# Kernel tuning notes

Hardware: AMD Instinct MI355X
Metric: run time of the kernel (lower is better)

The kernel has to match this reference:

```python
import jax, jax.numpy as jnp
import numpy as np
import math

DIM = 1024
H = 16
DH = DIM // H
B = 2
L = 1024


def setup_inputs() -> dict:
    key = jax.random.key(0)
    ks = jax.random.split(key, 8)
    s = 1.0 / math.sqrt(DIM)
    return {
        "Q": jax.random.normal(ks[0], (B, L, DIM), jnp.float32),
        "K": jax.random.normal(ks[1], (B, L, DIM), jnp.float32),
        "mask_Q": jax.random.bernoulli(ks[2], 0.1, (B, L)),
        "mask_K": jax.random.bernoulli(ks[3], 0.1, (B, L)),
        "Wq": jax.random.normal(ks[4], (DIM, DIM), jnp.float32) * s,
        "Wk": jax.random.normal(ks[5], (DIM, DIM), jnp.float32) * s,
        "Wv": jax.random.normal(ks[6], (DIM, DIM), jnp.float32) * s,
        "Wo": jax.random.normal(ks[7], (DIM, DIM), jnp.float32) * s,
    }


def reference(Q, K, mask_Q, mask_K, Wq, Wk, Wv, Wo):
    # V defaults to K. Masked positions of inputs are zeroed first.
    Qz = jnp.where(mask_Q[:, :, None], 0.0, Q)
    Kz = jnp.where(mask_K[:, :, None], 0.0, K)
    Vz = Kz  # V = K, masked with mask_K

    # Projections (nn.Linear, no bias): y = x @ W.T
    Qp = jnp.einsum('bld,ed->ble', Qz, Wq)
    Kp = jnp.einsum('bld,ed->ble', Kz, Wk)
    Vp = jnp.einsum('bld,ed->ble', Vz, Wv)

    # split heads: [B, L, H, DH] -> per-head attention
    qh = Qp.reshape(B, L, H, DH)
    kh = Kp.reshape(B, L, H, DH)
    vh = Vp.reshape(B, L, H, DH)

    # NOTE: original scales by sqrt(dim) (full dim), not sqrt(dim_split)
    scores = jnp.einsum('bqhd,bkhd->bhqk', qh, kh) / math.sqrt(DIM)

    # outer-product validity mask: valid iff both q and k positions unmasked
    valid = (~mask_Q)[:, None, :, None] & (~mask_K)[:, None, None, :]  # [B,1,Lq,Lk]
    A = jnp.where(valid, scores, -1e38)
    A = jax.nn.softmax(A, axis=-1)
    A = jnp.where(valid, A, 0.0)

    O = jnp.einsum('bhqk,bkhd->bqhd', A, vh).reshape(B, L, DIM)
    # residual uses the PROJECTED Q (Q was reassigned to fc_q(Q) in torch)
    O = Qp + O
    # masked_forward(fc_o, ...): fc_o applied, masked query rows forced to 0
    ff = jax.nn.relu(jnp.where(mask_Q[:, :, None], 0.0, jnp.einsum('bld,ed->ble', O, Wo)))
    O = O + ff
    return O
```

## Files before the change

### kernel.cpp

```cpp
#include <hip/hip_runtime.h>
#include <hip/hip_bf16.h>


#define DEV __device__ __forceinline__

typedef __attribute__((ext_vector_type(8))) short bf16x8;
typedef __attribute__((ext_vector_type(4))) float f32x4;
typedef __hip_bfloat16 bf16;

DEV void glds16(const bf16* g, bf16* s) {
  __builtin_amdgcn_global_load_lds(
      (const __attribute__((address_space(1))) void*)g,
      (__attribute__((address_space(3))) void*)s, 16, 0, 0);
}

DEV unsigned short f2bu(float x) {
  __hip_bfloat16 b = __float2bfloat16(x);
  unsigned short u;
  __builtin_memcpy(&u, &b, 2);
  return u;
}

__global__ void normalize_masks(const unsigned char* mq_raw, const unsigned char* mk_raw,
                                unsigned char* outq, unsigned char* outk,
                                unsigned long long* qm64, unsigned long long* km64) {
  __shared__ int cnt;
  int t = threadIdx.x;
  if (t == 0) cnt = 0;
  __syncthreads();
  int c = 0;
  for (int i = t; i < 2048; i += 256) c += (mq_raw[i] != 0);
  atomicAdd(&cnt, c);
  __syncthreads();
  bool isByte = cnt > 128;
  for (int i = t; i < 2048; i += 256) {
    unsigned char q, k;
    if (isByte) {
      q = (mq_raw[i] != 0); k = (mk_raw[i] != 0);
    } else {
      q = (((const int*)mq_raw)[i] != 0); k = (((const int*)mk_raw)[i] != 0);
    }
    outq[i] = q; outk[i] = k;
  }
  __syncthreads();
  if (t < 64) {
    const unsigned char* src = (t < 32) ? outk : outq;
    int idx = t & 31;
    unsigned long long m = 0;
    for (int j = 0; j < 64; ++j)
      m |= (unsigned long long)(src[idx * 64 + j] != 0) << j;
    if (t < 32) km64[idx] = m; else qm64[idx] = m;
  }
}

__global__ __launch_bounds__(256) void cast_all(
    const float* __restrict__ Q, const float* __restrict__ K,
    const unsigned char* __restrict__ mq, const unsigned char* __restrict__ mk,
    const float* __restrict__ W0, const float* __restrict__ W1,
    const float* __restrict__ W2, const float* __restrict__ W3,
    bf16* __restrict__ Qz, bf16* __restrict__ Kz,
    bf16* __restrict__ o0, bf16* __restrict__ o1,
    bf16* __restrict__ o2, bf16* __restrict__ o3) {
  const int z = blockIdx.z;
  if (z < 2) {
    const float* X = z ? K : Q;
    const unsigned char* m = z ? mk : mq;
    bf16* out = z ? Kz : Qz;
    int i = (blockIdx.x * 256 + threadIdx.x) * 8;
    float4 v0 = *(const float4*)&X[i];
    float4 v1 = *(const float4*)&X[i + 4];
    if (m[i >> 10]) {
      v0 = make_float4(0.f, 0.f, 0.f, 0.f);
      v1 = make_float4(0.f, 0.f, 0.f, 0.f);
    }
    *(ushort4*)&out[i] = make_ushort4(f2bu(v0.x), f2bu(v0.y), f2bu(v0.z), f2bu(v0.w));
    *(ushort4*)&out[i + 4] = make_ushort4(f2bu(v1.x), f2bu(v1.y), f2bu(v1.z), f2bu(v1.w));
  } else {
    const float* X; bf16* out;
    switch (z) {
      case 2: X = W0; out = o0; break;
      case 3: X = W1; out = o1; break;
      case 4: X = W2; out = o2; break;
      default: X = W3; out = o3; break;
    }
    int i = (blockIdx.x * 256 + threadIdx.x) * 4;
    float4 v = *(const float4*)&X[i];
    *(ushort4*)&out[i] = make_ushort4(f2bu(v.x), f2bu(v.y), f2bu(v.z), f2bu(v.w));
  }
}

template <int MI, typename EPI>
DEV void gemm_core(const bf16* __restrict__ A, const bf16* __restrict__ W,
                   int K, int brow, int bcol, EPI&& epi) {
  constexpr int BM = MI * 32;
  __shared__ bf16 As[2][BM * 32];
  __shared__ bf16 Bs[2][128 * 32];
  const int t = threadIdx.x, l = t & 63, w = t >> 6;
  const int wr = w >> 1, wc = w & 1;
  const int rs = l >> 2;
  const int kcol = (l & 3) * 8;

  f32x4 acc[MI][4];
#pragma unroll
  for (int i = 0; i < MI; i++)
#pragma unroll
    for (int j = 0; j < 4; j++) acc[i][j] = (f32x4){0.f, 0.f, 0.f, 0.f};

  const int aoff = (wr * (MI * 16) + (l & 15)) * 32 + (l >> 4) * 8;
  const int boff = (wc * 64 + (l & 15)) * 32 + (l >> 4) * 8;

  auto stage = [&](int k0, int b_) {
    if constexpr (MI == 4) {
#pragma unroll
      for (int c = 0; c < 2; ++c)
        glds16(A + (size_t)(brow + w * 32 + c * 16 + rs) * K + k0 + kcol,
               &As[b_][w * 1024 + c * 512]);
    } else {
      glds16(A + (size_t)(brow + w * 16 + rs) * K + k0 + kcol, &As[b_][w * 512]);
    }
#pragma unroll
    for (int c = 0; c < 2; ++c)
      glds16(W + (size_t)(bcol + w * 32 + c * 16 + rs) * K + k0 + kcol,
             &Bs[b_][w * 1024 + c * 512]);
  };

  stage(0, 0);
  int buf = 0;
  for (int k0 = 0; k0 < K; k0 += 32) {
    __syncthreads();
    if (k0 + 32 < K) stage(k0 + 32, buf ^ 1);
    bf16x8 a[MI], b[4];
#pragma unroll
    for (int mi = 0; mi < MI; ++mi) a[mi] = *(const bf16x8*)&As[buf][aoff + mi * 512];
#pragma unroll
    for (int ni = 0; ni < 4; ++ni) b[ni] = *(const bf16x8*)&Bs[buf][boff + ni * 512];
#pragma unroll
    for (int mi = 0; mi < MI; ++mi)
#pragma unroll
      for (int ni = 0; ni < 4; ++ni)
        acc[mi][ni] = __builtin_amdgcn_mfma_f32_16x16x32_bf16(a[mi], b[ni], acc[mi][ni], 0, 0, 0);
    buf ^= 1;
  }

#pragma unroll
  for (int mi = 0; mi < MI; ++mi)
#pragma unroll
    for (int ni = 0; ni < 4; ++ni)
#pragma unroll
      for (int r = 0; r < 4; ++r) {
        int row = brow + wr * (MI * 16) + mi * 16 + (l >> 4) * 4 + r;
        int col = bcol + wc * 64 + ni * 16 + (l & 15);
        epi(row, col, acc[mi][ni][r]);
      }
}

__global__ __launch_bounds__(256) void proj_gemm(
    const bf16* __restrict__ Qz, const bf16* __restrict__ Kz,
    const bf16* __restrict__ Wq, const bf16* __restrict__ Wk, const bf16* __restrict__ Wv,
    float* __restrict__ Qpf, bf16* __restrict__ Qpb,
    bf16* __restrict__ Kpb, bf16* __restrict__ Vpb) {
  const int z = blockIdx.z;
  const int brow = blockIdx.x * 128, bcol = blockIdx.y * 128;
  if (z == 0) {
    gemm_core<4>(Qz, Wq, 1024, brow, bcol, [&](int row, int col, float v) {
      size_t idx = (size_t)row * 1024 + col;
      Qpf[idx] = v;
      Qpb[idx] = __float2bfloat16(v * 0.045084220f);
    });
  } else if (z == 1) {
    gemm_core<4>(Kz, Wk, 1024, brow, bcol, [&](int row, int col, float v) {
      Kpb[(size_t)row * 1024 + col] = __float2bfloat16(v);
    });
  } else {
    gemm_core<4>(Kz, Wv, 1024, brow, bcol, [&](int row, int col, float v) {
      Vpb[(size_t)row * 1024 + col] = __float2bfloat16(v);
    });
  }
}

__global__ __launch_bounds__(256) void final_gemm(
    const bf16* __restrict__ Ob, const bf16* __restrict__ Wo,
    float* __restrict__ out, const unsigned char* __restrict__ mq) {
  const int brow = blockIdx.x * 64, bcol = blockIdx.y * 128;
  gemm_core<2>(Ob, Wo, 1024, brow, bcol, [&](int row, int col, float v) {
    size_t idx = (size_t)row * 1024 + col;
    float ff = mq[row] ? 0.f : fmaxf(v, 0.f);
    out[idx] = out[idx] + ff;
  });
}

__global__ __launch_bounds__(256) void attn_fused(
    const bf16* __restrict__ Qpb, const bf16* __restrict__ Kpb, const bf16* __restrict__ Vpb,
    const float* __restrict__ Qpf,
    const unsigned long long* __restrict__ qm64, const unsigned long long* __restrict__ km64,
    float* __restrict__ Of, bf16* __restrict__ Ob) {
  __shared__ bf16 Klds[2][64 * 64];
  __shared__ bf16 Vt[64 * 72];

  const int t = threadIdx.x, l = t & 63, w = t >> 6;
  const int q = l & 15, g = l >> 4;
  const int f = blockIdx.x;
  const int bh = (f & 7) + 8 * ((f >> 3) & 3);
  const int qt = f >> 5;
  const int b = bh >> 4, h = bh & 15;
  const size_t bbase = (size_t)b * 1024;

  const int qg = qt * 64 + w * 16 + q;
  const bf16* qptr = Qpb + (bbase + qg) * 1024 + h * 64 + g * 8;
  const bf16x8 qb0 = *(const bf16x8*)qptr;
  const bf16x8 qb1 = *(const bf16x8*)(qptr + 32);

  float psum = 0.f;
  f32x4 oacc[4];
#pragma unroll
  for (int mf = 0; mf < 4; ++mf) oacc[mf] = (f32x4){0.f, 0.f, 0.f, 0.f};

  const int krow_s = l >> 3;
  const int kcol_s = ((l & 7) ^ krow_s) * 8;
  const int vk0 = 2 * (t & 31);
  const int vdc = t >> 5;

  union { uint4 v; unsigned short s[8]; } u0, u1;

  auto stageK = [&](int kt_, int b_) {
#pragma unroll
    for (int c = 0; c < 2; ++c) {
      int cw = w * 2 + c;
      glds16(Kpb + (bbase + kt_ * 64 + cw * 8 + krow_s) * 1024 + h * 64 + kcol_s,
             &Klds[b_][cw * 512]);
    }
  };
  auto loadV = [&](int kt_) {
    const bf16* g0 = Vpb + (bbase + kt_ * 64 + vk0) * 1024 + h * 64 + vdc * 8;
    u0.v = *(const uint4*)g0;
    u1.v = *(const uint4*)(g0 + 1024);
  };

  stageK(0, 0);
  loadV(0);
  int buf = 0;

  for (int kt = 0; kt < 16; ++kt) {
    const unsigned long long km = km64[b * 16 + kt];
    const unsigned long long mloc = km >> (4 * g);

    __syncthreads();

#pragma unroll
    for (int j = 0; j < 8; ++j) {
      unsigned int pk = (unsigned int)u0.s[j] | ((unsigned int)u1.s[j] << 16);
      *(unsigned int*)((char*)Vt + (vdc * 8 + j) * 144 + vk0 * 2) = pk;
    }

    f32x4 S[4];
#pragma unroll
    for (int mf = 0; mf < 4; ++mf) {
#pragma unroll
      for (int r = 0; r < 4; ++r)
        S[mf][r] = ((mloc >> (mf * 16 + r)) & 1ull) ? -1e30f : 0.f;
      const int row = mf * 16 + q;
      const int rowb = row * 128;
      const bf16x8 ka0 = *(const bf16x8*)((const char*)&Klds[buf][0] + rowb + ((g ^ (row & 7)) * 16));
      const bf16x8 ka1 = *(const bf16x8*)((const char*)&Klds[buf][0] + rowb + (((g + 4) ^ (row & 7)) * 16));
      S[mf] = __builtin_amdgcn_mfma_f32_16x16x32_bf16(ka0, qb0, S[mf], 0, 0, 0);
      S[mf] = __builtin_amdgcn_mfma_f32_16x16x32_bf16(ka1, qb1, S[mf], 0, 0, 0);
    }

    unsigned int lo[4], hi[4];
#pragma unroll
    for (int mf = 0; mf < 4; ++mf) {
      float p0 = exp2f(S[mf][0]), p1 = exp2f(S[mf][1]);
      float p2 = exp2f(S[mf][2]), p3 = exp2f(S[mf][3]);
      psum += (p0 + p1) + (p2 + p3);
      lo[mf] = (unsigned int)f2bu(p0) | ((unsigned int)f2bu(p1) << 16);
      hi[mf] = (unsigned int)f2bu(p2) | ((unsigned int)f2bu(p3) << 16);
    }

    __syncthreads();

    if (kt < 15) {
      stageK(kt + 1, buf ^ 1);
      loadV(kt + 1);
    }

    const int srcA = ((2 * g) & 3) * 16 + q;
    const int srcB = srcA + 16;
    const bool sel = (g >> 1) & 1;
#pragma unroll
    for (int ks = 0; ks < 2; ++ks) {
      unsigned int a0 = __shfl(lo[2 * ks], srcA), a1 = __shfl(hi[2 * ks], srcA);
      unsigned int a2 = __shfl(lo[2 * ks], srcB), a3 = __shfl(hi[2 * ks], srcB);
      unsigned int b0 = __shfl(lo[2 * ks + 1], srcA), b1 = __shfl(hi[2 * ks + 1], srcA);
      unsigned int b2 = __shfl(lo[2 * ks + 1], srcB), b3 = __shfl(hi[2 * ks + 1], srcB);
      uint4 pw;
      pw.x = sel ? b0 : a0; pw.y = sel ? b1 : a1;
      pw.z = sel ? b2 : a2; pw.w = sel ? b3 : a3;
      const bf16x8 pa = __builtin_bit_cast(bf16x8, pw);
#pragma unroll
      for (int mf = 0; mf < 4; ++mf) {
        const bf16x8 va = *(const bf16x8*)((const char*)Vt + (mf * 16 + q) * 144 + ks * 64 + g * 16);
        oacc[mf] = __builtin_amdgcn_mfma_f32_16x16x32_bf16(va, pa, oacc[mf], 0, 0, 0);
      }
    }
    buf ^= 1;
  }

  psum += __shfl_xor(psum, 16);
  psum += __shfl_xor(psum, 32);

  const unsigned long long qm = qm64[b * 16 + qt];
  const bool qvalid = !((qm >> (w * 16 + q)) & 1ull);
  const float inv = (qvalid && psum > 0.f) ? 1.f / psum : 0.f;
#pragma unroll
  for (int mf = 0; mf < 4; ++mf) {
    size_t idx = (bbase + qg) * 1024 + h * 64 + mf * 16 + g * 4;
    float4 qp = *(const float4*)&Qpf[idx];
    float4 val;
    val.x = qp.x + oacc[mf][0] * inv;
    val.y = qp.y + oacc[mf][1] * inv;
    val.z = qp.z + oacc[mf][2] * inv;
    val.w = qp.w + oacc[mf][3] * inv;
    *(float4*)&Of[idx] = val;
    *(ushort4*)&Ob[idx] = make_ushort4(f2bu(val.x), f2bu(val.y), f2bu(val.z), f2bu(val.w));
  }
}

extern "C" void kernel_launch(void* const* d_in, const int* in_sizes, int n_in,
                              void* d_out, int out_size, void* d_ws, size_t ws_size,
                              hipStream_t stream) {
  const float* Q = (const float*)d_in[0];
  const float* K = (const float*)d_in[1];
  const unsigned char* mQraw = (const unsigned char*)d_in[2];
  const unsigned char* mKraw = (const unsigned char*)d_in[3];
  const float* Wq = (const float*)d_in[4];
  const float* Wk = (const float*)d_in[5];
  const float* Wv = (const float*)d_in[6];
  const float* Wo = (const float*)d_in[7];
  float* out = (float*)d_out;

  char* ws = (char*)d_ws;
  const size_t MB = 1024 * 1024;
  bf16* Qz = (bf16*)(ws + 0);
  bf16* Kz = (bf16*)(ws + 4 * MB);
  bf16* Wqb = (bf16*)(ws + 8 * MB);
  bf16* Wkb = (bf16*)(ws + 10 * MB);
  bf16* Wvb = (bf16*)(ws + 12 * MB);
  bf16* Wob = (bf16*)(ws + 14 * MB);
  float* Qpf = (float*)(ws + 16 * MB);
  bf16* Qpb = (bf16*)(ws + 24 * MB);
  bf16* Kpb = (bf16*)(ws + 28 * MB);
  bf16* Vpb = (bf16*)(ws + 32 * MB);
  bf16* Ob = (bf16*)(ws + 36 * MB);
  unsigned char* mqn = (unsigned char*)(ws + 40 * MB);
  unsigned char* mkn = mqn + 2048;
  unsigned long long* km64 = (unsigned long long*)(ws + 40 * MB + 4096);
  unsigned long long* qm64 = km64 + 32;

  normalize_masks<<<1, 256, 0, stream>>>(mQraw, mKraw, mqn, mkn, qm64, km64);

  dim3 gc(1024, 1, 6);
  cast_all<<<gc, 256, 0, stream>>>(Q, K, mqn, mkn, Wq, Wk, Wv, Wo,
                                   Qz, Kz, Wqb, Wkb, Wvb, Wob);

  dim3 gp(16, 8, 3);
  proj_gemm<<<gp, 256, 0, stream>>>(Qz, Kz, Wqb, Wkb, Wvb, Qpf, Qpb, Kpb, Vpb);

  attn_fused<<<512, 256, 0, stream>>>(Qpb, Kpb, Vpb, Qpf, qm64, km64, out, Ob);

  dim3 gf(32, 8);
  final_gemm<<<gf, 256, 0, stream>>>(Ob, Wob, out, mqn);
}
```

Measured before the change: 112.1 us.

## Retile GEMMs for more blocks and drop fp32 projected-Q buffer

The shared GEMM core is generalised to MI x NI tiles, where each wave owns a column strip instead of sharing a 2x2 warp grid. The projection GEMM moves to 64x128 tiles (768 blocks) and the output GEMM to 64x64 tiles (512 blocks), which raises occupancy and wave count on the many-CU GPU. The fp32 copy of the projected Q is no longer written. The attention epilogue instead rebuilds the residual from the scaled bf16 Q, cutting global write and read traffic at the cost of bf16 precision in the residual path. Smaller tiles lower per-block data reuse and add more redundant loads of A and W.

```diff
diff --git a/kernel.cpp b/kernel.cpp
--- a/kernel.cpp
+++ b/kernel.cpp
@@ -19,6 +19,13 @@
   unsigned short u;
   __builtin_memcpy(&u, &b, 2);
   return u;
+}
+
+DEV float bu2f(unsigned short u) {
+  unsigned int v = (unsigned int)u << 16;
+  float f;
+  __builtin_memcpy(&f, &v, 4);
+  return f;
 }
 
 __global__ void normalize_masks(const unsigned char* mq_raw, const unsigned char* mk_raw,
@@ -89,55 +96,52 @@
   }
 }
 
-template <int MI, typename EPI>
+template <int MI, int NI, typename EPI>
 DEV void gemm_core(const bf16* __restrict__ A, const bf16* __restrict__ W,
                    int K, int brow, int bcol, EPI&& epi) {
-  constexpr int BM = MI * 32;
-  __shared__ bf16 As[2][BM * 32];
-  __shared__ bf16 Bs[2][128 * 32];
+  __shared__ bf16 As[2 * MI * 512];
+  __shared__ bf16 Bs[2 * NI * 2048];
   const int t = threadIdx.x, l = t & 63, w = t >> 6;
-  const int wr = w >> 1, wc = w & 1;
   const int rs = l >> 2;
   const int kcol = (l & 3) * 8;
 
-  f32x4 acc[MI][4];
+  f32x4 acc[MI][NI];
 #pragma unroll
   for (int i = 0; i < MI; i++)
 #pragma unroll
-    for (int j = 0; j < 4; j++) acc[i][j] = (f32x4){0.f, 0.f, 0.f, 0.f};
-
-  const int aoff = (wr * (MI * 16) + (l & 15)) * 32 + (l >> 4) * 8;
-  const int boff = (wc * 64 + (l & 15)) * 32 + (l >> 4) * 8;
+    for (int j = 0; j < NI; j++) acc[i][j] = (f32x4){0.f, 0.f, 0.f, 0.f};
 
   auto stage = [&](int k0, int b_) {
-    if constexpr (MI == 4) {
-#pragma unroll
-      for (int c = 0; c < 2; ++c)
-        glds16(A + (size_t)(brow + w * 32 + c * 16 + rs) * K + k0 + kcol,
-               &As[b_][w * 1024 + c * 512]);
-    } else {
-      glds16(A + (size_t)(brow + w * 16 + rs) * K + k0 + kcol, &As[b_][w * 512]);
-    }
-#pragma unroll
-    for (int c = 0; c < 2; ++c)
-      glds16(W + (size_t)(bcol + w * 32 + c * 16 + rs) * K + k0 + kcol,
-             &Bs[b_][w * 1024 + c * 512]);
+#pragma unroll
+    for (int i = 0; i < MI; ++i)
+      if ((i & 3) == w)
+        glds16(A + (size_t)(brow + i * 16 + rs) * K + k0 + kcol,
+               &As[b_ * MI * 512 + i * 512]);
+#pragma unroll
+    for (int c = 0; c < NI; ++c)
+      glds16(W + (size_t)(bcol + (w * NI + c) * 16 + rs) * K + k0 + kcol,
+             &Bs[b_ * NI * 2048 + (w * NI + c) * 512]);
   };
+
+  const int aoff0 = (l & 15) * 32 + (l >> 4) * 8;
+  const int boff0 = (w * NI * 16 + (l & 15)) * 32 + (l >> 4) * 8;
 
   stage(0, 0);
   int buf = 0;
   for (int k0 = 0; k0 < K; k0 += 32) {
     __syncthreads();
     if (k0 + 32 < K) stage(k0 + 32, buf ^ 1);
-    bf16x8 a[MI], b[4];
-#pragma unroll
-    for (int mi = 0; mi < MI; ++mi) a[mi] = *(const bf16x8*)&As[buf][aoff + mi * 512];
-#pragma unroll
-    for (int ni = 0; ni < 4; ++ni) b[ni] = *(const bf16x8*)&Bs[buf][boff + ni * 512];
+    bf16x8 a[MI], b[NI];
 #pragma unroll
     for (int mi = 0; mi < MI; ++mi)
-#pragma unroll
-      for (int ni = 0; ni < 4; ++ni)
+      a[mi] = *(const bf16x8*)&As[buf * MI * 512 + aoff0 + mi * 512];
+#pragma unroll
+    for (int ni = 0; ni < NI; ++ni)
+      b[ni] = *(const bf16x8*)&Bs[buf * NI * 2048 + boff0 + ni * 512];
+#pragma unroll
+    for (int mi = 0; mi < MI; ++mi)
+#pragma unroll
+      for (int ni = 0; ni < NI; ++ni)
         acc[mi][ni] = __builtin_amdgcn_mfma_f32_16x16x32_bf16(a[mi], b[ni], acc[mi][ni], 0, 0, 0);
     buf ^= 1;
   }
@@ -145,11 +149,11 @@
 #pragma unroll
   for (int mi = 0; mi < MI; ++mi)
 #pragma unroll
-    for (int ni = 0; ni < 4; ++ni)
+    for (int ni = 0; ni < NI; ++ni)
 #pragma unroll
       for (int r = 0; r < 4; ++r) {
-        int row = brow + wr * (MI * 16) + mi * 16 + (l >> 4) * 4 + r;
-        int col = bcol + wc * 64 + ni * 16 + (l & 15);
+        int row = brow + mi * 16 + (l >> 4) * 4 + r;
+        int col = bcol + (w * NI + ni) * 16 + (l & 15);
         epi(row, col, acc[mi][ni][r]);
       }
 }
@@ -157,33 +161,24 @@
 __global__ __launch_bounds__(256) void proj_gemm(
     const bf16* __restrict__ Qz, const bf16* __restrict__ Kz,
     const bf16* __restrict__ Wq, const bf16* __restrict__ Wk, const bf16* __restrict__ Wv,
-    float* __restrict__ Qpf, bf16* __restrict__ Qpb,
-    bf16* __restrict__ Kpb, bf16* __restrict__ Vpb) {
+    bf16* __restrict__ Qpb, bf16* __restrict__ Kpb, bf16* __restrict__ Vpb) {
   const int z = blockIdx.z;
-  const int brow = blockIdx.x * 128, bcol = blockIdx.y * 128;
-  if (z == 0) {
-    gemm_core<4>(Qz, Wq, 1024, brow, bcol, [&](int row, int col, float v) {
-      size_t idx = (size_t)row * 1024 + col;
-      Qpf[idx] = v;
-      Qpb[idx] = __float2bfloat16(v * 0.045084220f);
-    });
-  } else if (z == 1) {
-    gemm_core<4>(Kz, Wk, 1024, brow, bcol, [&](int row, int col, float v) {
-      Kpb[(size_t)row * 1024 + col] = __float2bfloat16(v);
-    });
-  } else {
-    gemm_core<4>(Kz, Wv, 1024, brow, bcol, [&](int row, int col, float v) {
-      Vpb[(size_t)row * 1024 + col] = __float2bfloat16(v);
-    });
-  }
+  const int brow = blockIdx.x * 64, bcol = blockIdx.y * 128;
+  const bf16* A = (z == 0) ? Qz : Kz;
+  const bf16* W = (z == 0) ? Wq : ((z == 1) ? Wk : Wv);
+  bf16* dst = (z == 0) ? Qpb : ((z == 1) ? Kpb : Vpb);
+  const float scale = (z == 0) ? 0.045084220f : 1.0f;
+  gemm_core<4, 2>(A, W, 1024, brow, bcol, [&](int row, int col, float v) {
+    dst[((size_t)row << 10) + col] = __float2bfloat16(v * scale);
+  });
 }
 
 __global__ __launch_bounds__(256) void final_gemm(
     const bf16* __restrict__ Ob, const bf16* __restrict__ Wo,
     float* __restrict__ out, const unsigned char* __restrict__ mq) {
-  const int brow = blockIdx.x * 64, bcol = blockIdx.y * 128;
-  gemm_core<2>(Ob, Wo, 1024, brow, bcol, [&](int row, int col, float v) {
-    size_t idx = (size_t)row * 1024 + col;
+  const int brow = blockIdx.x * 64, bcol = blockIdx.y * 64;
+  gemm_core<4, 1>(Ob, Wo, 1024, brow, bcol, [&](int row, int col, float v) {
+    size_t idx = ((size_t)row << 10) + col;
     float ff = mq[row] ? 0.f : fmaxf(v, 0.f);
     out[idx] = out[idx] + ff;
   });
@@ -191,7 +186,6 @@
 
 __global__ __launch_bounds__(256) void attn_fused(
     const bf16* __restrict__ Qpb, const bf16* __restrict__ Kpb, const bf16* __restrict__ Vpb,
-    const float* __restrict__ Qpf,
     const unsigned long long* __restrict__ qm64, const unsigned long long* __restrict__ km64,
     float* __restrict__ Of, bf16* __restrict__ Ob) {
   __shared__ bf16 Klds[2][64 * 64];
@@ -311,15 +305,16 @@
   const unsigned long long qm = qm64[b * 16 + qt];
   const bool qvalid = !((qm >> (w * 16 + q)) & 1ull);
   const float inv = (qvalid && psum > 0.f) ? 1.f / psum : 0.f;
+  const float RQ = 22.180709777918f;
 #pragma unroll
   for (int mf = 0; mf < 4; ++mf) {
     size_t idx = (bbase + qg) * 1024 + h * 64 + mf * 16 + g * 4;
-    float4 qp = *(const float4*)&Qpf[idx];
+    ushort4 q4 = *(const ushort4*)&Qpb[idx];
     float4 val;
-    val.x = qp.x + oacc[mf][0] * inv;
-    val.y = qp.y + oacc[mf][1] * inv;
-    val.z = qp.z + oacc[mf][2] * inv;
-    val.w = qp.w + oacc[mf][3] * inv;
+    val.x = bu2f(q4.x) * RQ + oacc[mf][0] * inv;
+    val.y = bu2f(q4.y) * RQ + oacc[mf][1] * inv;
+    val.z = bu2f(q4.z) * RQ + oacc[mf][2] * inv;
+    val.w = bu2f(q4.w) * RQ + oacc[mf][3] * inv;
     *(float4*)&Of[idx] = val;
     *(ushort4*)&Ob[idx] = make_ushort4(f2bu(val.x), f2bu(val.y), f2bu(val.z), f2bu(val.w));
   }
@@ -346,14 +341,13 @@
   bf16* Wkb = (bf16*)(ws + 10 * MB);
   bf16* Wvb = (bf16*)(ws + 12 * MB);
   bf16* Wob = (bf16*)(ws + 14 * MB);
-  float* Qpf = (float*)(ws + 16 * MB);
-  bf16* Qpb = (bf16*)(ws + 24 * MB);
-  bf16* Kpb = (bf16*)(ws + 28 * MB);
-  bf16* Vpb = (bf16*)(ws + 32 * MB);
-  bf16* Ob = (bf16*)(ws + 36 * MB);
-  unsigned char* mqn = (unsigned char*)(ws + 40 * MB);
+  bf16* Qpb = (bf16*)(ws + 16 * MB);
+  bf16* Kpb = (bf16*)(ws + 20 * MB);
+  bf16* Vpb = (bf16*)(ws + 24 * MB);
+  bf16* Ob  = (bf16*)(ws + 28 * MB);
+  unsigned char* mqn = (unsigned char*)(ws + 32 * MB);
   unsigned char* mkn = mqn + 2048;
-  unsigned long long* km64 = (unsigned long long*)(ws + 40 * MB + 4096);
+  unsigned long long* km64 = (unsigned long long*)(ws + 32 * MB + 4096);
   unsigned long long* qm64 = km64 + 32;
 
   normalize_masks<<<1, 256, 0, stream>>>(mQraw, mKraw, mqn, mkn, qm64, km64);
@@ -362,11 +356,11 @@
   cast_all<<<gc, 256, 0, stream>>>(Q, K, mqn, mkn, Wq, Wk, Wv, Wo,
                                    Qz, Kz, Wqb, Wkb, Wvb, Wob);
 
-  dim3 gp(16, 8, 3);
-  proj_gemm<<<gp, 256, 0, stream>>>(Qz, Kz, Wqb, Wkb, Wvb, Qpf, Qpb, Kpb, Vpb);
-
-  attn_fused<<<512, 256, 0, stream>>>(Qpb, Kpb, Vpb, Qpf, qm64, km64, out, Ob);
-
-  dim3 gf(32, 8);
+  dim3 gp(32, 8, 3);
+  proj_gemm<<<gp, 256, 0, stream>>>(Qz, Kz, Wqb, Wkb, Wvb, Qpb, Kpb, Vpb);
+
+  attn_fused<<<512, 256, 0, stream>>>(Qpb, Kpb, Vpb, qm64, km64, out, Ob);
+
+  dim3 gf(32, 16);
   final_gemm<<<gf, 256, 0, stream>>>(Ob, Wob, out, mqn);
 }
```

After: 96.54 us. 1.16x faster.
